# Kernel optimization log

Measured on AMD Instinct MI355X. Metric: run time of the kernel, lower is better.

## Reference

```python
import jax, jax.numpy as jnp
import numpy as np

DT = 1.0


def setup_inputs() -> dict:
    key = jax.random.key(0)
    k1, k2 = jax.random.split(key)
    B, L, P = 32, 8192, 128
    x = jax.random.normal(k1, (B, L, P), dtype=jnp.float32)
    # CustomLinearLayer weight (relu applied in forward when training=True)
    w = jax.random.uniform(k2, (P,), dtype=jnp.float32)
    return {"x": x, "w": w}


def _binary_operator(q_i, q_j):
    # combine (A, Bu) pairs for the diagonal linear recurrence h_t = A*h_{t-1} + Bu_t
    A_i, b_i = q_i
    A_j, b_j = q_j
    return (A_j * A_i, A_j * b_i + b_j)


def reference(x, w):
    # diagonal RNN: h_{t} = h_{t-1} + dt * (x_t - relu(w) * h_{t-1})
    #             = (1 - dt*relu(w)) * h_{t-1} + dt * x_t,   h_0 = 0
    wa = jax.nn.relu(w)                      # (P,)
    A = jnp.broadcast_to(1.0 - DT * wa, x.shape)  # (B, L, P) constant over time
    b = DT * x                                # (B, L, P)
    _, hidden = jax.lax.associative_scan(_binary_operator, (A, b), axis=1)
    return hidden  # (B, L, P), return_sequences=True
```

## Files before the change

kernel.cpp:

```cpp
#include <hip/hip_runtime.h>


typedef float f4 __attribute__((ext_vector_type(4)));

#define BB 32
#define LL 8192
#define PP 128
#define TPB 256
#define CHUNK 16
#define GPB 8
#define BSTEPS (CHUNK * GPB)
#define BPR (LL / BSTEPS)
#define GRID (BB * BPR)

__device__ __forceinline__ f4 make_a4(const float* __restrict__ w, int l) {
  const f4 w4 = reinterpret_cast<const f4*>(w)[l];
  f4 a4;
  a4.x = 1.0f - fmaxf(w4.x, 0.0f);
  a4.y = 1.0f - fmaxf(w4.y, 0.0f);
  a4.z = 1.0f - fmaxf(w4.z, 0.0f);
  a4.w = 1.0f - fmaxf(w4.w, 0.0f);
  return a4;
}

__global__ __launch_bounds__(TPB) void k1_aggs(
    const float* __restrict__ x, const float* __restrict__ w,
    float* __restrict__ gf ,
    float* __restrict__ agg ) {
  const int tid = threadIdx.x;
  const int g = tid >> 5;
  const int l = tid & 31;
  const int b = blockIdx.x / BPR;
  const int s = blockIdx.x % BPR;

  const f4 a4 = make_a4(w, l);

  const f4* xv = reinterpret_cast<const f4*>(x) +
                 ((size_t)b * LL + (size_t)s * BSTEPS + (size_t)g * CHUNK) * (PP / 4) + l;
  f4 h = (f4)(0.0f);
#pragma unroll
  for (int t = 0; t < CHUNK; ++t) {
    const f4 v = xv[(size_t)t * (PP / 4)];
    h.x = fmaf(a4.x, h.x, v.x);
    h.y = fmaf(a4.y, h.y, v.y);
    h.z = fmaf(a4.z, h.z, v.z);
    h.w = fmaf(a4.w, h.w, v.w);
  }

  reinterpret_cast<f4*>(gf)[(((size_t)b * BPR + s) * GPB + g) * (PP / 4) + l] = h;

  __shared__ float sf[GPB][PP];
  reinterpret_cast<f4*>(&sf[g][0])[l] = h;
  __syncthreads();

  if (tid < PP) {
    const int p = tid;
    const float a = 1.0f - fmaxf(w[p], 0.0f);
    float a16 = a;
#pragma unroll
    for (int i = 0; i < 4; ++i) a16 *= a16;
    float bf = 0.f;
#pragma unroll
    for (int g2 = 0; g2 < GPB; ++g2) bf = fmaf(a16, bf, sf[g2][p]);
    agg[((size_t)b * BPR + s) * PP + p] = bf;
  }
}

__global__ __launch_bounds__(TPB) void k2_emit(
    const float* __restrict__ x, const float* __restrict__ w,
    const float* __restrict__ gf ,
    const float* __restrict__ agg ,
    float* __restrict__ out) {
  const int tid = threadIdx.x;
  const int g = tid >> 5;
  const int l = tid & 31;
  const int b = blockIdx.x / BPR;
  const int s = blockIdx.x % BPR;

  __shared__ float seed[GPB][PP];

  if (tid < PP) {
    const int p = tid;
    const float a = 1.0f - fmaxf(w[p], 0.0f);
    float a16 = a;
#pragma unroll
    for (int i = 0; i < 4; ++i) a16 *= a16;
    float a128 = a16;
#pragma unroll
    for (int i = 0; i < 3; ++i) a128 *= a128;

    float hh = 0.f;
    const float* bp = agg + (size_t)b * BPR * PP + p;
    int j = 0;
    for (; j + 8 <= s; j += 8) {
      const float v0 = bp[(size_t)(j + 0) * PP];
      const float v1 = bp[(size_t)(j + 1) * PP];
      const float v2 = bp[(size_t)(j + 2) * PP];
      const float v3 = bp[(size_t)(j + 3) * PP];
      const float v4 = bp[(size_t)(j + 4) * PP];
      const float v5 = bp[(size_t)(j + 5) * PP];
      const float v6 = bp[(size_t)(j + 6) * PP];
      const float v7 = bp[(size_t)(j + 7) * PP];
      hh = fmaf(a128, hh, v0);
      hh = fmaf(a128, hh, v1);
      hh = fmaf(a128, hh, v2);
      hh = fmaf(a128, hh, v3);
      hh = fmaf(a128, hh, v4);
      hh = fmaf(a128, hh, v5);
      hh = fmaf(a128, hh, v6);
      hh = fmaf(a128, hh, v7);
    }
    for (; j < s; ++j) hh = fmaf(a128, hh, bp[(size_t)j * PP]);

    const float* gp = gf + ((size_t)b * BPR + s) * GPB * PP + p;
#pragma unroll
    for (int g2 = 0; g2 < GPB; ++g2) {
      seed[g2][p] = hh;
      hh = fmaf(a16, hh, gp[(size_t)g2 * PP]);
    }
  }
  __syncthreads();

  const f4 a4 = make_a4(w, l);
  f4 h = reinterpret_cast<const f4*>(&seed[g][0])[l];

  const size_t off = ((size_t)b * LL + (size_t)s * BSTEPS + (size_t)g * CHUNK) * (PP / 4) + l;
  const f4* xv = reinterpret_cast<const f4*>(x) + off;
  f4* ov = reinterpret_cast<f4*>(out) + off;
#pragma unroll
  for (int t = 0; t < CHUNK; ++t) {
    const f4 v = __builtin_nontemporal_load(&xv[(size_t)t * (PP / 4)]);
    h.x = fmaf(a4.x, h.x, v.x);
    h.y = fmaf(a4.y, h.y, v.y);
    h.z = fmaf(a4.z, h.z, v.z);
    h.w = fmaf(a4.w, h.w, v.w);
    __builtin_nontemporal_store(h, &ov[(size_t)t * (PP / 4)]);
  }
}

extern "C" void kernel_launch(void* const* d_in, const int* in_sizes, int n_in,
                              void* d_out, int out_size, void* d_ws, size_t ws_size,
                              hipStream_t stream) {
  const float* x = (const float*)d_in[0];
  const float* w = (const float*)d_in[1];
  float* out = (float*)d_out;
  float* gf = (float*)d_ws;
  float* agg = gf + (size_t)BB * BPR * GPB * PP;

  k1_aggs<<<GRID, TPB, 0, stream>>>(x, w, gf, agg);
  k2_emit<<<GRID, TPB, 0, stream>>>(x, w, gf, agg, out);
}
```

Measured before the change: 74.02 us.

## Recompute per-group chunk sums in emit kernel instead of storing them

```diff
diff --git a/kernel.cpp b/kernel.cpp
--- a/kernel.cpp
+++ b/kernel.cpp
@@ -25,7 +25,6 @@
 
 __global__ __launch_bounds__(TPB) void k1_aggs(
     const float* __restrict__ x, const float* __restrict__ w,
-    float* __restrict__ gf ,
     float* __restrict__ agg ) {
   const int tid = threadIdx.x;
   const int g = tid >> 5;
@@ -47,8 +46,6 @@
     h.w = fmaf(a4.w, h.w, v.w);
   }
 
-  reinterpret_cast<f4*>(gf)[(((size_t)b * BPR + s) * GPB + g) * (PP / 4) + l] = h;
-
   __shared__ float sf[GPB][PP];
   reinterpret_cast<f4*>(&sf[g][0])[l] = h;
   __syncthreads();
@@ -68,7 +65,6 @@
 
 __global__ __launch_bounds__(TPB) void k2_emit(
     const float* __restrict__ x, const float* __restrict__ w,
-    const float* __restrict__ gf ,
     const float* __restrict__ agg ,
     float* __restrict__ out) {
   const int tid = threadIdx.x;
@@ -77,19 +73,29 @@
   const int b = blockIdx.x / BPR;
   const int s = blockIdx.x % BPR;
 
-  __shared__ float seed[GPB][PP];
+  const f4 a4 = make_a4(w, l);
 
+  const size_t off = ((size_t)b * LL + (size_t)s * BSTEPS + (size_t)g * CHUNK) * (PP / 4) + l;
+  const f4* xv = reinterpret_cast<const f4*>(x) + off;
+
+  f4 xr[CHUNK];
+#pragma unroll
+  for (int t = 0; t < CHUNK; ++t)
+    xr[t] = __builtin_nontemporal_load(&xv[(size_t)t * (PP / 4)]);
+
+  float hh = 0.f;
+  float a16_s = 0.f;
   if (tid < PP) {
     const int p = tid;
     const float a = 1.0f - fmaxf(w[p], 0.0f);
     float a16 = a;
 #pragma unroll
     for (int i = 0; i < 4; ++i) a16 *= a16;
+    a16_s = a16;
     float a128 = a16;
 #pragma unroll
     for (int i = 0; i < 3; ++i) a128 *= a128;
 
-    float hh = 0.f;
     const float* bp = agg + (size_t)b * BPR * PP + p;
     int j = 0;
     for (; j + 8 <= s; j += 8) {
@@ -111,29 +117,41 @@
       hh = fmaf(a128, hh, v7);
     }
     for (; j < s; ++j) hh = fmaf(a128, hh, bp[(size_t)j * PP]);
+  }
 
-    const float* gp = gf + ((size_t)b * BPR + s) * GPB * PP + p;
+  __shared__ float sf[GPB][PP];
+  __shared__ float seed[GPB][PP];
+  {
+    f4 h = (f4)(0.0f);
+#pragma unroll
+    for (int t = 0; t < CHUNK; ++t) {
+      h.x = fmaf(a4.x, h.x, xr[t].x);
+      h.y = fmaf(a4.y, h.y, xr[t].y);
+      h.z = fmaf(a4.z, h.z, xr[t].z);
+      h.w = fmaf(a4.w, h.w, xr[t].w);
+    }
+    reinterpret_cast<f4*>(&sf[g][0])[l] = h;
+  }
+  __syncthreads();
+
+  if (tid < PP) {
+    const int p = tid;
 #pragma unroll
     for (int g2 = 0; g2 < GPB; ++g2) {
       seed[g2][p] = hh;
-      hh = fmaf(a16, hh, gp[(size_t)g2 * PP]);
+      hh = fmaf(a16_s, hh, sf[g2][p]);
     }
   }
   __syncthreads();
 
-  const f4 a4 = make_a4(w, l);
   f4 h = reinterpret_cast<const f4*>(&seed[g][0])[l];
-
-  const size_t off = ((size_t)b * LL + (size_t)s * BSTEPS + (size_t)g * CHUNK) * (PP / 4) + l;
-  const f4* xv = reinterpret_cast<const f4*>(x) + off;
   f4* ov = reinterpret_cast<f4*>(out) + off;
 #pragma unroll
   for (int t = 0; t < CHUNK; ++t) {
-    const f4 v = __builtin_nontemporal_load(&xv[(size_t)t * (PP / 4)]);
-    h.x = fmaf(a4.x, h.x, v.x);
-    h.y = fmaf(a4.y, h.y, v.y);
-    h.z = fmaf(a4.z, h.z, v.z);
-    h.w = fmaf(a4.w, h.w, v.w);
+    h.x = fmaf(a4.x, h.x, xr[t].x);
+    h.y = fmaf(a4.y, h.y, xr[t].y);
+    h.z = fmaf(a4.z, h.z, xr[t].z);
+    h.w = fmaf(a4.w, h.w, xr[t].w);
     __builtin_nontemporal_store(h, &ov[(size_t)t * (PP / 4)]);
   }
 }
@@ -144,9 +162,8 @@
   const float* x = (const float*)d_in[0];
   const float* w = (const float*)d_in[1];
   float* out = (float*)d_out;
-  float* gf = (float*)d_ws;
-  float* agg = gf + (size_t)BB * BPR * GPB * PP;
+  float* agg = (float*)d_ws;
 
-  k1_aggs<<<GRID, TPB, 0, stream>>>(x, w, gf, agg);
-  k2_emit<<<GRID, TPB, 0, stream>>>(x, w, gf, agg, out);
+  k1_aggs<<<GRID, TPB, 0, stream>>>(x, w, agg);
+  k2_emit<<<GRID, TPB, 0, stream>>>(x, w, agg, out);
 }
```

Result: faster. 68.00 us (-8.1%).
